# Kernel optimization log

Measured on AMD Instinct MI355X. Metric: run time of the kernel, lower is better.

The kernel has to match this reference:

```python
import jax, jax.numpy as jnp
import numpy as np
import math

N, D, DV, B = 8192, 128, 128, 64
PHI_EPS = 1e-4
NORM_EPS = 1e-8


def _make_omega(dimv=128, dimqk=128, seed=0):
    # Faithful to FavorAttention._omega: QR of uniform blocks, rows renormalized
    # by norms of uniform rows, then transposed -> shape (dimqk, dimv).
    rng = np.random.default_rng(seed)
    nblocks = dimv // dimqk
    blocks = []
    for _ in range(nblocks):
        q, _ = np.linalg.qr(rng.random((dimqk, dimqk)))
        blocks.append(q.T)
    missing = dimv - nblocks * dimqk
    if missing > 0:
        q, _ = np.linalg.qr(rng.random((dimqk, dimqk)))
        blocks.append(q.T[:missing])
    norm = np.linalg.norm(rng.random((dimv, dimqk)), axis=1, keepdims=True)
    return (norm * np.vstack(blocks)).T.astype(np.float32)


def setup_inputs() -> dict:
    key = jax.random.key(0)
    kq, kk, kv, kb = jax.random.split(key, 4)
    Q = jax.random.normal(kq, (N, D), dtype=jnp.float32)
    K = jax.random.normal(kk, (N, D), dtype=jnp.float32)
    V = jax.random.normal(kv, (N, DV), dtype=jnp.float32)
    batch_seg = jnp.sort(jax.random.randint(kb, (N,), 0, B)).astype(jnp.int64)
    omega = jnp.asarray(_make_omega(128, 128))
    return {"Q": Q, "K": K, "V": V, "omega": omega,
            "batch_seg": batch_seg, "num_batch": B}


def _phi(x, omega, is_query, batch_seg, num_batch):
    d = x.shape[-1]
    m = omega.shape[-1]
    U = (x / d ** 0.25) @ omega                              # [n, m]
    h = jnp.sum(x * x, axis=-1, keepdims=True) / (2.0 * d ** 0.5)
    if is_query:
        maximum = jnp.max(U, axis=-1, keepdims=True)         # per-row max
    else:
        # per-segment max of masked U; original masks off-segment entries with 0,
        # so the effective per-segment max is clamped at 0.
        row_max = jnp.max(U, axis=-1)                        # [n]
        seg_max = jax.ops.segment_max(row_max, batch_seg, num_segments=num_batch)
        seg_max = jnp.maximum(seg_max, 0.0)
        maximum = seg_max[batch_seg][:, None]                # [n, 1]
    return (jnp.exp(U - h - maximum) + PHI_EPS) / math.sqrt(m)


def reference(Q, K, V, omega, batch_seg, num_batch):
    # FAVOR+ linear attention with segment-wise (per-molecule) normalization.
    Qp = _phi(Q, omega, True, batch_seg, num_batch)          # [n, m]
    Kp = _phi(K, omega, False, batch_seg, num_batch)         # [n, m]
    # norm_i = Qp_i . sum_{j in seg(i)} Kp_j  + eps
    Ksum = jax.ops.segment_sum(Kp, batch_seg, num_segments=num_batch)  # [B, m]
    norm = jnp.einsum('nm,nm->n', Qp, Ksum[batch_seg]) + NORM_EPS      # [n]
    # S_b = sum_{j in b} Kp_j (outer) V_j ; equals the masked (K Q^T)^T V of the
    # original, without materializing the n x n matrix.
    S = jax.ops.segment_sum(Kp[:, :, None] * V[:, None, :], batch_seg,
                            num_segments=num_batch)          # [B, m, dv]
    out = jnp.einsum('nm,nmd->nd', Qp, S[batch_seg]) / norm[:, None]
    return out
```

## Files before the change

### kernel.cpp

```cpp
#include <hip/hip_runtime.h>
#include <math.h>


#define NROWS 8192
#define DIM   128
#define NSEG  64

#define INV_D4      0.29730177875068026f
#define H_SCALE     0.04419417382415922f
#define INV_SQRT_M  0.08838834764831845f
#define PHI_EPS_F   1e-4f
#define NORM_EPS_F  1e-8f

__global__ __launch_bounds__(256, 2) void k_phi(
    const float* __restrict__ Q, const float* __restrict__ K,
    const float* __restrict__ omega, const int* __restrict__ seg,
    float* __restrict__ Qp, float* __restrict__ UK,
    float* __restrict__ hK, int* __restrict__ segmax)
{
    __shared__ float om[DIM * DIM];
    __shared__ float xs[4][8][DIM];

    const int t = threadIdx.x;
    {
        const float4* src = (const float4*)omega;
        float4* dst = (float4*)om;
#pragma unroll
        for (int i = 0; i < 16; ++i) dst[t + i * 256] = src[t + i * 256];
    }

    const int w    = t >> 6;
    const int lane = t & 63;
    const int rg   = lane >> 5;
    const int cl   = lane & 31;
    const int rowbase = blockIdx.x * 32 + w * 8;
    const bool isQ = rowbase < NROWS;
    const float* X = isQ ? (Q + (size_t)rowbase * DIM)
                         : (K + (size_t)(rowbase - NROWS) * DIM);

    float hpart[4];
    {
        const float4* xg = (const float4*)X;
        float4* xd = (float4*)&xs[w][0][0];
#pragma unroll
        for (int i = 0; i < 4; ++i) {
            float4 v = xg[i * 64 + lane];
            hpart[i] = v.x * v.x + v.y * v.y + v.z * v.z + v.w * v.w;
            float4 sv;
            sv.x = v.x * INV_D4; sv.y = v.y * INV_D4;
            sv.z = v.z * INV_D4; sv.w = v.w * INV_D4;
            xd[i * 64 + lane] = sv;
        }
    }
    float hrow[4];
#pragma unroll
    for (int i = 0; i < 4; ++i) {
        float v = hpart[i];
#pragma unroll
        for (int m = 1; m < 32; m <<= 1) v += __shfl_xor(v, m, 64);
        hrow[i] = v * H_SCALE;
    }
    __syncthreads();

    float4 acc[4];
#pragma unroll
    for (int i = 0; i < 4; ++i) acc[i] = make_float4(0.f, 0.f, 0.f, 0.f);

#pragma unroll 4
    for (int d = 0; d < DIM; d += 4) {
        const float4 o0 = *(const float4*)&om[(d + 0) * DIM + cl * 4];
        const float4 o1 = *(const float4*)&om[(d + 1) * DIM + cl * 4];
        const float4 o2 = *(const float4*)&om[(d + 2) * DIM + cl * 4];
        const float4 o3 = *(const float4*)&om[(d + 3) * DIM + cl * 4];
#pragma unroll
        for (int i = 0; i < 4; ++i) {
            const float4 xv = *(const float4*)&xs[w][2 * i + rg][d];
            acc[i].x = fmaf(xv.x, o0.x, fmaf(xv.y, o1.x, fmaf(xv.z, o2.x, fmaf(xv.w, o3.x, acc[i].x))));
            acc[i].y = fmaf(xv.x, o0.y, fmaf(xv.y, o1.y, fmaf(xv.z, o2.y, fmaf(xv.w, o3.y, acc[i].y))));
            acc[i].z = fmaf(xv.x, o0.z, fmaf(xv.y, o1.z, fmaf(xv.z, o2.z, fmaf(xv.w, o3.z, acc[i].z))));
            acc[i].w = fmaf(xv.x, o0.w, fmaf(xv.y, o1.w, fmaf(xv.z, o2.w, fmaf(xv.w, o3.w, acc[i].w))));
        }
    }

#pragma unroll
    for (int i = 0; i < 4; ++i) {
        const int row = rowbase + 2 * i + rg;
        const float4 a = acc[i];
        float mx = fmaxf(fmaxf(a.x, a.y), fmaxf(a.z, a.w));
#pragma unroll
        for (int m = 1; m < 32; m <<= 1) mx = fmaxf(mx, __shfl_xor(mx, m, 64));
        if (isQ) {
            const float b = hrow[i] + mx;
            float4 o;
            o.x = (__expf(a.x - b) + PHI_EPS_F) * INV_SQRT_M;
            o.y = (__expf(a.y - b) + PHI_EPS_F) * INV_SQRT_M;
            o.z = (__expf(a.z - b) + PHI_EPS_F) * INV_SQRT_M;
            o.w = (__expf(a.w - b) + PHI_EPS_F) * INV_SQRT_M;
            *(float4*)&Qp[(size_t)row * DIM + cl * 4] = o;
        } else {
            const int krow = row - NROWS;
            *(float4*)&UK[(size_t)krow * DIM + cl * 4] = a;
            if (cl == 0) {
                hK[krow] = hrow[i];
                if (mx > 0.0f)
                    atomicMax(&segmax[seg[krow]], __float_as_int(mx));
            }
        }
    }
}

__global__ __launch_bounds__(256, 4) void k_accum(
    const float* __restrict__ UK, const float* __restrict__ hK,
    const float* __restrict__ V, const int* __restrict__ seg,
    const float* __restrict__ segmax,
    float* __restrict__ S, float* __restrict__ Ksum)
{
    __shared__ float kp[32][32];
    __shared__ float vv[32][32];

    const int t = threadIdx.x;
    const int sid  = blockIdx.x >> 4;
    const int tile = blockIdx.x & 15;
    const int tm = (tile >> 2) * 32;
    const int tv = (tile & 3) * 32;

    int start, end;
    {
        int a = 0, b = NROWS;
        while (a < b) { int m = (a + b) >> 1; if (seg[m] < sid) a = m + 1; else b = m; }
        start = a;
        b = NROWS;
        while (a < b) { int m = (a + b) >> 1; if (seg[m] < sid + 1) a = m + 1; else b = m; }
        end = a;
    }

    const float smax = segmax[sid];
    const int rs = t >> 3;
    const int cs = (t & 7) * 4;
    const int ty = t >> 4;
    const int tx = t & 15;

    float a00 = 0.f, a01 = 0.f, a10 = 0.f, a11 = 0.f;
    float4 ksl = make_float4(0.f, 0.f, 0.f, 0.f);

    for (int j = start; j < end; j += 32) {
        const int row = j + rs;
        float4 kpv = make_float4(0.f, 0.f, 0.f, 0.f);
        float4 vvv = make_float4(0.f, 0.f, 0.f, 0.f);
        if (row < end) {
            const float4 u = *(const float4*)&UK[(size_t)row * DIM + tm + cs];
            const float h = hK[row] + smax;
            kpv.x = (__expf(u.x - h) + PHI_EPS_F) * INV_SQRT_M;
            kpv.y = (__expf(u.y - h) + PHI_EPS_F) * INV_SQRT_M;
            kpv.z = (__expf(u.z - h) + PHI_EPS_F) * INV_SQRT_M;
            kpv.w = (__expf(u.w - h) + PHI_EPS_F) * INV_SQRT_M;
            vvv = *(const float4*)&V[(size_t)row * DIM + tv + cs];
        }
        __syncthreads();
        *(float4*)&kp[rs][cs] = kpv;
        *(float4*)&vv[rs][cs] = vvv;
        ksl.x += kpv.x; ksl.y += kpv.y; ksl.z += kpv.z; ksl.w += kpv.w;
        __syncthreads();
#pragma unroll
        for (int k = 0; k < 32; ++k) {
            const float2 ka = *(const float2*)&kp[k][ty * 2];
            const float2 vb = *(const float2*)&vv[k][tx * 2];
            a00 = fmaf(ka.x, vb.x, a00);
            a01 = fmaf(ka.x, vb.y, a01);
            a10 = fmaf(ka.y, vb.x, a10);
            a11 = fmaf(ka.y, vb.y, a11);
        }
    }

    float* Sseg = S + (size_t)sid * DIM * DIM;
    {
        float2 r0; r0.x = a00; r0.y = a01;
        float2 r1; r1.x = a10; r1.y = a11;
        *(float2*)&Sseg[(tm + 2 * ty + 0) * DIM + tv + 2 * tx] = r0;
        *(float2*)&Sseg[(tm + 2 * ty + 1) * DIM + tv + 2 * tx] = r1;
    }

    __syncthreads();
    *(float4*)&kp[rs][cs] = ksl;
    __syncthreads();
    if (tv == 0 && t < 32) {
        float s = 0.f;
#pragma unroll
        for (int r = 0; r < 32; ++r) s += kp[r][t];
        Ksum[sid * DIM + tm + t] = s;
    }
}

__global__ __launch_bounds__(256, 2) void k_out(
    const float* __restrict__ Qp, const float* __restrict__ S,
    const float* __restrict__ Ksum, const int* __restrict__ seg,
    float* __restrict__ out)
{
    __shared__ float Sl[DIM * DIM];
    __shared__ float Ks[DIM];
    __shared__ float qb[4][4 * DIM];

    const int t = threadIdx.x;
    const int w = t >> 6, lane = t & 63;
    const int rg = lane >> 5, cl = lane & 31;
    const int base = blockIdx.x * 16;
    const int bend = base + 16;

    int i = base;
    while (i < bend) {
        const int sid = seg[i];
        int e = i + 1;
        while (e < bend && seg[e] == sid) ++e;

        __syncthreads();
        {
            const float4* src = (const float4*)(S + (size_t)sid * DIM * DIM);
            float4* dst = (float4*)Sl;
#pragma unroll
            for (int q = 0; q < 16; ++q) dst[t + q * 256] = src[t + q * 256];
            if (t < DIM) Ks[t] = Ksum[sid * DIM + t];
        }
        __syncthreads();

        for (int r0 = i + w * 4; r0 < e; r0 += 16) {
            {
                float2* dst = (float2*)&qb[w][0];
#pragma unroll
                for (int q = 0; q < 4; ++q) {
                    const int idx = q * 64 + lane;
                    const int grow = min(r0 + (idx >> 6), NROWS - 1);
                    dst[idx] = ((const float2*)(Qp + (size_t)grow * DIM))[idx & 63];
                }
            }
            const float* qA = &qb[w][(rg * 2 + 0) * DIM];
            const float* qB = &qb[w][(rg * 2 + 1) * DIM];
            float4 accA = make_float4(0.f, 0.f, 0.f, 0.f);
            float4 accB = make_float4(0.f, 0.f, 0.f, 0.f);
            float nA = 0.f, nB = 0.f;

#pragma unroll 4
            for (int m = 0; m < DIM; m += 4) {
                const float4 qa4 = *(const float4*)&qA[m];
                const float4 qb4 = *(const float4*)&qB[m];
                const float4 ks4 = *(const float4*)&Ks[m];
                const float qav[4] = {qa4.x, qa4.y, qa4.z, qa4.w};
                const float qbv[4] = {qb4.x, qb4.y, qb4.z, qb4.w};
                const float ksv[4] = {ks4.x, ks4.y, ks4.z, ks4.w};
#pragma unroll
                for (int k = 0; k < 4; ++k) {
                    const float4 s4 = *(const float4*)&Sl[(m + k) * DIM + cl * 4];
                    accA.x = fmaf(qav[k], s4.x, accA.x);
                    accA.y = fmaf(qav[k], s4.y, accA.y);
                    accA.z = fmaf(qav[k], s4.z, accA.z);
                    accA.w = fmaf(qav[k], s4.w, accA.w);
                    accB.x = fmaf(qbv[k], s4.x, accB.x);
                    accB.y = fmaf(qbv[k], s4.y, accB.y);
                    accB.z = fmaf(qbv[k], s4.z, accB.z);
                    accB.w = fmaf(qbv[k], s4.w, accB.w);
                    nA = fmaf(qav[k], ksv[k], nA);
                    nB = fmaf(qbv[k], ksv[k], nB);
                }
            }

            const int rA = r0 + rg * 2, rB = rA + 1;
            if (rA < e) {
                const float inv = 1.0f / (nA + NORM_EPS_F);
                float4 o; o.x = accA.x * inv; o.y = accA.y * inv;
                o.z = accA.z * inv; o.w = accA.w * inv;
                *(float4*)&out[(size_t)rA * DIM + cl * 4] = o;
            }
            if (rB < e) {
                const float inv = 1.0f / (nB + NORM_EPS_F);
                float4 o; o.x = accB.x * inv; o.y = accB.y * inv;
                o.z = accB.z * inv; o.w = accB.w * inv;
                *(float4*)&out[(size_t)rB * DIM + cl * 4] = o;
            }
        }
        i = e;
    }
}

extern "C" void kernel_launch(void* const* d_in, const int* in_sizes, int n_in,
                              void* d_out, int out_size, void* d_ws, size_t ws_size,
                              hipStream_t stream)
{
    const float* Q     = (const float*)d_in[0];
    const float* K     = (const float*)d_in[1];
    const float* V     = (const float*)d_in[2];
    const float* omega = (const float*)d_in[3];
    const int*   seg   = (const int*)d_in[4];
    float* out = (float*)d_out;

    float* ws     = (float*)d_ws;
    float* S      = ws;
    float* Ksum   = S + (size_t)NSEG * DIM * DIM;
    float* segmax = Ksum + NSEG * DIM;
    float* Qp     = segmax + NSEG;
    float* UK     = Qp + (size_t)NROWS * DIM;
    float* hK     = UK + (size_t)NROWS * DIM;

    hipMemsetAsync(segmax, 0, NSEG * sizeof(float), stream);

    hipLaunchKernelGGL(k_phi, dim3(512), dim3(256), 0, stream,
                       Q, K, omega, seg, Qp, UK, hK, (int*)segmax);
    hipLaunchKernelGGL(k_accum, dim3(NSEG * 16), dim3(256), 0, stream,
                       UK, hK, V, seg, segmax, S, Ksum);
    hipLaunchKernelGGL(k_out, dim3(512), dim3(256), 0, stream,
                       Qp, S, Ksum, seg, out);
}
```

Baseline: 153.5 us.

## Drop LDS staging of omega and S; read from global with smaller row tiles

k_phi no longer copies the whole 64KB omega matrix into shared memory. Each block now handles 16 rows instead of 32, with twice as many blocks, and omega is read directly from global/L2. k_out no longer stages each segment's 64KB S matrix in LDS per segment run; each thread pair reads S rows for its own segment from global and computes the norm with a shuffle reduction. The aim is to cut LDS footprint and per-block staging cost and raise occupancy, at the price of repeated global/L2 reads of omega and S with no reuse across rows in a block.

After: 164.1 us. 1.07x slower.

```diff
diff --git a/kernel.cpp b/kernel.cpp
--- a/kernel.cpp
+++ b/kernel.cpp
@@ -7,104 +7,104 @@
 #define NSEG  64
 
 #define INV_D4      0.29730177875068026f
-#define H_SCALE     0.04419417382415922f
 #define INV_SQRT_M  0.08838834764831845f
 #define PHI_EPS_F   1e-4f
 #define NORM_EPS_F  1e-8f
 
-__global__ __launch_bounds__(256, 2) void k_phi(
+__global__ __launch_bounds__(256, 4) void k_phi(
     const float* __restrict__ Q, const float* __restrict__ K,
     const float* __restrict__ omega, const int* __restrict__ seg,
     float* __restrict__ Qp, float* __restrict__ UK,
     float* __restrict__ hK, int* __restrict__ segmax)
 {
-    __shared__ float om[DIM * DIM];
-    __shared__ float xs[4][8][DIM];
+    __shared__ float xs[16][DIM];
 
     const int t = threadIdx.x;
-    {
-        const float4* src = (const float4*)omega;
-        float4* dst = (float4*)om;
-#pragma unroll
-        for (int i = 0; i < 16; ++i) dst[t + i * 256] = src[t + i * 256];
-    }
-
-    const int w    = t >> 6;
-    const int lane = t & 63;
-    const int rg   = lane >> 5;
-    const int cl   = lane & 31;
-    const int rowbase = blockIdx.x * 32 + w * 8;
-    const bool isQ = rowbase < NROWS;
-    const float* X = isQ ? (Q + (size_t)rowbase * DIM)
-                         : (K + (size_t)(rowbase - NROWS) * DIM);
-
-    float hpart[4];
+    const int bid = blockIdx.x;
+    const bool isQ = bid < 512;
+    const int rowbase = (isQ ? bid : bid - 512) * 16;
+    const float* X = (isQ ? Q : K) + (size_t)rowbase * DIM;
+
     {
         const float4* xg = (const float4*)X;
-        float4* xd = (float4*)&xs[w][0][0];
-#pragma unroll
-        for (int i = 0; i < 4; ++i) {
-            float4 v = xg[i * 64 + lane];
-            hpart[i] = v.x * v.x + v.y * v.y + v.z * v.z + v.w * v.w;
-            float4 sv;
-            sv.x = v.x * INV_D4; sv.y = v.y * INV_D4;
-            sv.z = v.z * INV_D4; sv.w = v.w * INV_D4;
-            xd[i * 64 + lane] = sv;
-        }
-    }
-    float hrow[4];
-#pragma unroll
-    for (int i = 0; i < 4; ++i) {
-        float v = hpart[i];
-#pragma unroll
-        for (int m = 1; m < 32; m <<= 1) v += __shfl_xor(v, m, 64);
-        hrow[i] = v * H_SCALE;
-    }
-    __syncthreads();
-
-    float4 acc[4];
-#pragma unroll
-    for (int i = 0; i < 4; ++i) acc[i] = make_float4(0.f, 0.f, 0.f, 0.f);
-
-#pragma unroll 4
+        float4* xd = (float4*)&xs[0][0];
+#pragma unroll
+        for (int s = 0; s < 2; ++s) {
+            float4 v = xg[t + s * 256];
+            v.x *= INV_D4; v.y *= INV_D4; v.z *= INV_D4; v.w *= INV_D4;
+            xd[t + s * 256] = v;
+        }
+    }
+    __syncthreads();
+
+    const int w = t >> 6, lane = t & 63;
+    const int rg = lane >> 5, cl = lane & 31;
+    const int rA = w * 4 + rg * 2, rB = rA + 1;
+
+    float hA, hB;
+    {
+        const float4 a = *(const float4*)&xs[rA][cl * 4];
+        const float4 b = *(const float4*)&xs[rB][cl * 4];
+        float pa = a.x * a.x + a.y * a.y + a.z * a.z + a.w * a.w;
+        float pb = b.x * b.x + b.y * b.y + b.z * b.z + b.w * b.w;
+#pragma unroll
+        for (int m = 1; m < 32; m <<= 1) {
+            pa += __shfl_xor(pa, m, 64);
+            pb += __shfl_xor(pb, m, 64);
+        }
+        hA = 0.5f * pa; hB = 0.5f * pb;
+    }
+
+    float4 accA = make_float4(0.f, 0.f, 0.f, 0.f);
+    float4 accB = make_float4(0.f, 0.f, 0.f, 0.f);
+
+#pragma unroll 2
     for (int d = 0; d < DIM; d += 4) {
-        const float4 o0 = *(const float4*)&om[(d + 0) * DIM + cl * 4];
-        const float4 o1 = *(const float4*)&om[(d + 1) * DIM + cl * 4];
-        const float4 o2 = *(const float4*)&om[(d + 2) * DIM + cl * 4];
-        const float4 o3 = *(const float4*)&om[(d + 3) * DIM + cl * 4];
-#pragma unroll
-        for (int i = 0; i < 4; ++i) {
-            const float4 xv = *(const float4*)&xs[w][2 * i + rg][d];
-            acc[i].x = fmaf(xv.x, o0.x, fmaf(xv.y, o1.x, fmaf(xv.z, o2.x, fmaf(xv.w, o3.x, acc[i].x))));
-            acc[i].y = fmaf(xv.x, o0.y, fmaf(xv.y, o1.y, fmaf(xv.z, o2.y, fmaf(xv.w, o3.y, acc[i].y))));
-            acc[i].z = fmaf(xv.x, o0.z, fmaf(xv.y, o1.z, fmaf(xv.z, o2.z, fmaf(xv.w, o3.z, acc[i].z))));
-            acc[i].w = fmaf(xv.x, o0.w, fmaf(xv.y, o1.w, fmaf(xv.z, o2.w, fmaf(xv.w, o3.w, acc[i].w))));
-        }
-    }
-
-#pragma unroll
-    for (int i = 0; i < 4; ++i) {
-        const int row = rowbase + 2 * i + rg;
-        const float4 a = acc[i];
-        float mx = fmaxf(fmaxf(a.x, a.y), fmaxf(a.z, a.w));
-#pragma unroll
-        for (int m = 1; m < 32; m <<= 1) mx = fmaxf(mx, __shfl_xor(mx, m, 64));
-        if (isQ) {
-            const float b = hrow[i] + mx;
-            float4 o;
-            o.x = (__expf(a.x - b) + PHI_EPS_F) * INV_SQRT_M;
-            o.y = (__expf(a.y - b) + PHI_EPS_F) * INV_SQRT_M;
-            o.z = (__expf(a.z - b) + PHI_EPS_F) * INV_SQRT_M;
-            o.w = (__expf(a.w - b) + PHI_EPS_F) * INV_SQRT_M;
-            *(float4*)&Qp[(size_t)row * DIM + cl * 4] = o;
-        } else {
-            const int krow = row - NROWS;
-            *(float4*)&UK[(size_t)krow * DIM + cl * 4] = a;
-            if (cl == 0) {
-                hK[krow] = hrow[i];
-                if (mx > 0.0f)
-                    atomicMax(&segmax[seg[krow]], __float_as_int(mx));
-            }
+        const float4 o0 = *(const float4*)&omega[(size_t)(d + 0) * DIM + cl * 4];
+        const float4 o1 = *(const float4*)&omega[(size_t)(d + 1) * DIM + cl * 4];
+        const float4 o2 = *(const float4*)&omega[(size_t)(d + 2) * DIM + cl * 4];
+        const float4 o3 = *(const float4*)&omega[(size_t)(d + 3) * DIM + cl * 4];
+        const float4 xa = *(const float4*)&xs[rA][d];
+        const float4 xb = *(const float4*)&xs[rB][d];
+        accA.x = fmaf(xa.x, o0.x, fmaf(xa.y, o1.x, fmaf(xa.z, o2.x, fmaf(xa.w, o3.x, accA.x))));
+        accA.y = fmaf(xa.x, o0.y, fmaf(xa.y, o1.y, fmaf(xa.z, o2.y, fmaf(xa.w, o3.y, accA.y))));
+        accA.z = fmaf(xa.x, o0.z, fmaf(xa.y, o1.z, fmaf(xa.z, o2.z, fmaf(xa.w, o3.z, accA.z))));
+        accA.w = fmaf(xa.x, o0.w, fmaf(xa.y, o1.w, fmaf(xa.z, o2.w, fmaf(xa.w, o3.w, accA.w))));
+        accB.x = fmaf(xb.x, o0.x, fmaf(xb.y, o1.x, fmaf(xb.z, o2.x, fmaf(xb.w, o3.x, accB.x))));
+        accB.y = fmaf(xb.x, o0.y, fmaf(xb.y, o1.y, fmaf(xb.z, o2.y, fmaf(xb.w, o3.y, accB.y))));
+        accB.z = fmaf(xb.x, o0.z, fmaf(xb.y, o1.z, fmaf(xb.z, o2.z, fmaf(xb.w, o3.z, accB.z))));
+        accB.w = fmaf(xb.x, o0.w, fmaf(xb.y, o1.w, fmaf(xb.z, o2.w, fmaf(xb.w, o3.w, accB.w))));
+    }
+
+    float mA = fmaxf(fmaxf(accA.x, accA.y), fmaxf(accA.z, accA.w));
+    float mB = fmaxf(fmaxf(accB.x, accB.y), fmaxf(accB.z, accB.w));
+#pragma unroll
+    for (int m = 1; m < 32; m <<= 1) {
+        mA = fmaxf(mA, __shfl_xor(mA, m, 64));
+        mB = fmaxf(mB, __shfl_xor(mB, m, 64));
+    }
+
+    const int gA = rowbase + rA, gB = rowbase + rB;
+    if (isQ) {
+        const float bA = hA + mA, bB = hB + mB;
+        float4 eA, eB;
+        eA.x = (__expf(accA.x - bA) + PHI_EPS_F) * INV_SQRT_M;
+        eA.y = (__expf(accA.y - bA) + PHI_EPS_F) * INV_SQRT_M;
+        eA.z = (__expf(accA.z - bA) + PHI_EPS_F) * INV_SQRT_M;
+        eA.w = (__expf(accA.w - bA) + PHI_EPS_F) * INV_SQRT_M;
+        eB.x = (__expf(accB.x - bB) + PHI_EPS_F) * INV_SQRT_M;
+        eB.y = (__expf(accB.y - bB) + PHI_EPS_F) * INV_SQRT_M;
+        eB.z = (__expf(accB.z - bB) + PHI_EPS_F) * INV_SQRT_M;
+        eB.w = (__expf(accB.w - bB) + PHI_EPS_F) * INV_SQRT_M;
+        *(float4*)&Qp[(size_t)gA * DIM + cl * 4] = eA;
+        *(float4*)&Qp[(size_t)gB * DIM + cl * 4] = eB;
+    } else {
+        *(float4*)&UK[(size_t)gA * DIM + cl * 4] = accA;
+        *(float4*)&UK[(size_t)gB * DIM + cl * 4] = accB;
+        if (cl == 0) {
+            hK[gA] = hA; hK[gB] = hB;
+            if (mA > 0.f) atomicMax(&segmax[seg[gA]], __float_as_int(mA));
+            if (mB > 0.f) atomicMax(&segmax[seg[gB]], __float_as_int(mB));
         }
     }
 }
@@ -112,7 +112,7 @@
 __global__ __launch_bounds__(256, 4) void k_accum(
     const float* __restrict__ UK, const float* __restrict__ hK,
     const float* __restrict__ V, const int* __restrict__ seg,
-    const float* __restrict__ segmax,
+    const float* __restrict__ segmaxf,
     float* __restrict__ S, float* __restrict__ Ksum)
 {
     __shared__ float kp[32][32];
@@ -128,13 +128,12 @@
     {
         int a = 0, b = NROWS;
         while (a < b) { int m = (a + b) >> 1; if (seg[m] < sid) a = m + 1; else b = m; }
-        start = a;
-        b = NROWS;
+        start = a; b = NROWS;
         while (a < b) { int m = (a + b) >> 1; if (seg[m] < sid + 1) a = m + 1; else b = m; }
         end = a;
     }
 
-    const float smax = segmax[sid];
+    const float smax = segmaxf[sid];
     const int rs = t >> 3;
     const int cs = (t & 7) * 4;
     const int ty = t >> 4;
@@ -191,93 +190,79 @@
     }
 }
 
-__global__ __launch_bounds__(256, 2) void k_out(
+__global__ __launch_bounds__(256, 4) void k_out(
     const float* __restrict__ Qp, const float* __restrict__ S,
     const float* __restrict__ Ksum, const int* __restrict__ seg,
     float* __restrict__ out)
 {
-    __shared__ float Sl[DIM * DIM];
-    __shared__ float Ks[DIM];
-    __shared__ float qb[4][4 * DIM];
+    __shared__ float qs[16][DIM];
 
     const int t = threadIdx.x;
+    const int rowbase = blockIdx.x * 16;
+
+    {
+        const float4* xg = (const float4*)(Qp + (size_t)rowbase * DIM);
+        float4* xd = (float4*)&qs[0][0];
+#pragma unroll
+        for (int s = 0; s < 2; ++s) xd[t + s * 256] = xg[t + s * 256];
+    }
+    __syncthreads();
+
     const int w = t >> 6, lane = t & 63;
     const int rg = lane >> 5, cl = lane & 31;
-    const int base = blockIdx.x * 16;
-    const int bend = base + 16;
-
-    int i = base;
-    while (i < bend) {
-        const int sid = seg[i];
-        int e = i + 1;
-        while (e < bend && seg[e] == sid) ++e;
-
-        __syncthreads();
-        {
-            const float4* src = (const float4*)(S + (size_t)sid * DIM * DIM);
-            float4* dst = (float4*)Sl;
-#pragma unroll
-            for (int q = 0; q < 16; ++q) dst[t + q * 256] = src[t + q * 256];
-            if (t < DIM) Ks[t] = Ksum[sid * DIM + t];
-        }
-        __syncthreads();
-
-        for (int r0 = i + w * 4; r0 < e; r0 += 16) {
-            {
-                float2* dst = (float2*)&qb[w][0];
-#pragma unroll
-                for (int q = 0; q < 4; ++q) {
-                    const int idx = q * 64 + lane;
-                    const int grow = min(r0 + (idx >> 6), NROWS - 1);
-                    dst[idx] = ((const float2*)(Qp + (size_t)grow * DIM))[idx & 63];
-                }
-            }
-            const float* qA = &qb[w][(rg * 2 + 0) * DIM];
-            const float* qB = &qb[w][(rg * 2 + 1) * DIM];
-            float4 accA = make_float4(0.f, 0.f, 0.f, 0.f);
-            float4 accB = make_float4(0.f, 0.f, 0.f, 0.f);
-            float nA = 0.f, nB = 0.f;
-
-#pragma unroll 4
-            for (int m = 0; m < DIM; m += 4) {
-                const float4 qa4 = *(const float4*)&qA[m];
-                const float4 qb4 = *(const float4*)&qB[m];
-                const float4 ks4 = *(const float4*)&Ks[m];
-                const float qav[4] = {qa4.x, qa4.y, qa4.z, qa4.w};
-                const float qbv[4] = {qb4.x, qb4.y, qb4.z, qb4.w};
-                const float ksv[4] = {ks4.x, ks4.y, ks4.z, ks4.w};
-#pragma unroll
-                for (int k = 0; k < 4; ++k) {
-                    const float4 s4 = *(const float4*)&Sl[(m + k) * DIM + cl * 4];
-                    accA.x = fmaf(qav[k], s4.x, accA.x);
-                    accA.y = fmaf(qav[k], s4.y, accA.y);
-                    accA.z = fmaf(qav[k], s4.z, accA.z);
-                    accA.w = fmaf(qav[k], s4.w, accA.w);
-                    accB.x = fmaf(qbv[k], s4.x, accB.x);
-                    accB.y = fmaf(qbv[k], s4.y, accB.y);
-                    accB.z = fmaf(qbv[k], s4.z, accB.z);
-                    accB.w = fmaf(qbv[k], s4.w, accB.w);
-                    nA = fmaf(qav[k], ksv[k], nA);
-                    nB = fmaf(qbv[k], ksv[k], nB);
-                }
-            }
-
-            const int rA = r0 + rg * 2, rB = rA + 1;
-            if (rA < e) {
-                const float inv = 1.0f / (nA + NORM_EPS_F);
-                float4 o; o.x = accA.x * inv; o.y = accA.y * inv;
-                o.z = accA.z * inv; o.w = accA.w * inv;
-                *(float4*)&out[(size_t)rA * DIM + cl * 4] = o;
-            }
-            if (rB < e) {
-                const float inv = 1.0f / (nB + NORM_EPS_F);
-                float4 o; o.x = accB.x * inv; o.y = accB.y * inv;
-                o.z = accB.z * inv; o.w = accB.w * inv;
-                *(float4*)&out[(size_t)rB * DIM + cl * 4] = o;
-            }
-        }
-        i = e;
-    }
+    const int rA = w * 4 + rg * 2, rB = rA + 1;
+    const int gA = rowbase + rA, gB = rowbase + rB;
+    const int sA = seg[gA], sB = seg[gB];
+    const float* SA = S + (size_t)sA * DIM * DIM;
+    const float* SB = S + (size_t)sB * DIM * DIM;
+
+    float nA, nB;
+    {
+        const float4 qa = *(const float4*)&qs[rA][cl * 4];
+        const float4 qb = *(const float4*)&qs[rB][cl * 4];
+        const float4 ka = *(const float4*)&Ksum[sA * DIM + cl * 4];
+        const float4 kb = *(const float4*)&Ksum[sB * DIM + cl * 4];
+        float pa = qa.x * ka.x + qa.y * ka.y + qa.z * ka.z + qa.w * ka.w;
+        float pb = qb.x * kb.x + qb.y * kb.y + qb.z * kb.z + qb.w * kb.w;
+#pragma unroll
+        for (int m = 1; m < 32; m <<= 1) {
+            pa += __shfl_xor(pa, m, 64);
+            pb += __shfl_xor(pb, m, 64);
+        }
+        nA = pa + NORM_EPS_F; nB = pb + NORM_EPS_F;
+    }
+
+    float4 accA = make_float4(0.f, 0.f, 0.f, 0.f);
+    float4 accB = make_float4(0.f, 0.f, 0.f, 0.f);
+
+#pragma unroll 2
+    for (int m = 0; m < DIM; m += 4) {
+        const float4 qa = *(const float4*)&qs[rA][m];
+        const float4 qb = *(const float4*)&qs[rB][m];
+        const float4 a0 = *(const float4*)&SA[(size_t)(m + 0) * DIM + cl * 4];
+        const float4 a1 = *(const float4*)&SA[(size_t)(m + 1) * DIM + cl * 4];
+        const float4 a2 = *(const float4*)&SA[(size_t)(m + 2) * DIM + cl * 4];
+        const float4 a3 = *(const float4*)&SA[(size_t)(m + 3) * DIM + cl * 4];
+        const float4 b0 = *(const float4*)&SB[(size_t)(m + 0) * DIM + cl * 4];
+        const float4 b1 = *(const float4*)&SB[(size_t)(m + 1) * DIM + cl * 4];
+        const float4 b2 = *(const float4*)&SB[(size_t)(m + 2) * DIM + cl * 4];
+        const float4 b3 = *(const float4*)&SB[(size_t)(m + 3) * DIM + cl * 4];
+        accA.x = fmaf(qa.x, a0.x, fmaf(qa.y, a1.x, fmaf(qa.z, a2.x, fmaf(qa.w, a3.x, accA.x))));
+        accA.y = fmaf(qa.x, a0.y, fmaf(qa.y, a1.y, fmaf(qa.z, a2.y, fmaf(qa.w, a3.y, accA.y))));
+        accA.z = fmaf(qa.x, a0.z, fmaf(qa.y, a1.z, fmaf(qa.z, a2.z, fmaf(qa.w, a3.z, accA.z))));
+        accA.w = fmaf(qa.x, a0.w, fmaf(qa.y, a1.w, fmaf(qa.z, a2.w, fmaf(qa.w, a3.w, accA.w))));
+        accB.x = fmaf(qb.x, b0.x, fmaf(qb.y, b1.x, fmaf(qb.z, b2.x, fmaf(qb.w, b3.x, accB.x))));
+        accB.y = fmaf(qb.x, b0.y, fmaf(qb.y, b1.y, fmaf(qb.z, b2.y, fmaf(qb.w, b3.y, accB.y))));
+        accB.z = fmaf(qb.x, b0.z, fmaf(qb.y, b1.z, fmaf(qb.z, b2.z, fmaf(qb.w, b3.z, accB.z))));
+        accB.w = fmaf(qb.x, b0.w, fmaf(qb.y, b1.w, fmaf(qb.z, b2.w, fmaf(qb.w, b3.w, accB.w))));
+    }
+
+    const float iA = 1.0f / nA, iB = 1.0f / nB;
+    float4 oA, oB;
+    oA.x = accA.x * iA; oA.y = accA.y * iA; oA.z = accA.z * iA; oA.w = accA.w * iA;
+    oB.x = accB.x * iB; oB.y = accB.y * iB; oB.z = accB.z * iB; oB.w = accB.w * iB;
+    *(float4*)&out[(size_t)gA * DIM + cl * 4] = oA;
+    *(float4*)&out[(size_t)gB * DIM + cl * 4] = oB;
 }
 
 extern "C" void kernel_launch(void* const* d_in, const int* in_sizes, int n_in,
@@ -291,20 +276,20 @@
     const int*   seg   = (const int*)d_in[4];
     float* out = (float*)d_out;
 
-    float* ws     = (float*)d_ws;
-    float* S      = ws;
-    float* Ksum   = S + (size_t)NSEG * DIM * DIM;
-    float* segmax = Ksum + NSEG * DIM;
-    float* Qp     = segmax + NSEG;
-    float* UK     = Qp + (size_t)NROWS * DIM;
-    float* hK     = UK + (size_t)NROWS * DIM;
-
-    hipMemsetAsync(segmax, 0, NSEG * sizeof(float), stream);
-
-    hipLaunchKernelGGL(k_phi, dim3(512), dim3(256), 0, stream,
-                       Q, K, omega, seg, Qp, UK, hK, (int*)segmax);
+    float* ws      = (float*)d_ws;
+    float* S       = ws;
+    float* Ksum    = S + (size_t)NSEG * DIM * DIM;
+    float* segmaxf = Ksum + NSEG * DIM;
+    float* Qp      = segmaxf + NSEG;
+    float* UK      = Qp + (size_t)NROWS * DIM;
+    float* hK      = UK + (size_t)NROWS * DIM;
+
+    hipMemsetAsync(segmaxf, 0, NSEG * sizeof(float), stream);
+
+    hipLaunchKernelGGL(k_phi, dim3(1024), dim3(256), 0, stream,
+                       Q, K, omega, seg, Qp, UK, hK, (int*)segmaxf);
     hipLaunchKernelGGL(k_accum, dim3(NSEG * 16), dim3(256), 0, stream,
-                       UK, hK, V, seg, segmax, S, Ksum);
+                       UK, hK, V, seg, segmaxf, S, Ksum);
     hipLaunchKernelGGL(k_out, dim3(512), dim3(256), 0, stream,
                        Qp, S, Ksum, seg, out);
 }
```
